# Kernel tuning notes

Measured on AMD Instinct MI355X. Metric: run time of the kernel, lower is better.

## Reference

```python
import jax, jax.numpy as jnp
import numpy as np

LEAK = 0.95
THRESHOLD = 1.0
RESCALE = 2.0


def _xavier_uniform(key, shape, gain=2.0):
    fan_out, fan_in = shape
    bound = gain * np.sqrt(6.0 / (fan_in + fan_out))
    return jax.random.uniform(key, shape, jnp.float32, -bound, bound)


def setup_inputs() -> dict:
    key = jax.random.key(0)
    k_inp, k_w1, k_w2 = jax.random.split(key, 3)
    inp = jax.random.normal(k_inp, (8192, 784), jnp.float32)
    w1 = _xavier_uniform(k_w1, (800, 784))   # fc1.weight
    w2 = _xavier_uniform(k_w2, (10, 800))    # fc2.weight
    return {"inp": inp, "w1": w1, "w2": w2, "num_steps": 25}


@jax.custom_vjp
def spike_fn(x):
    return (x > 0).astype(x.dtype)

def _spike_fwd(x):
    return spike_fn(x), x

def _spike_bwd(x, g):
    # grad = g * 0.3 * relu(1 - |x|)  (surrogate BP)
    return (g * 0.3 * jnp.maximum(1.0 - jnp.abs(x), 0.0),)

spike_fn.defvjp(_spike_fwd, _spike_bwd)


def poisson_gen(key, inp):
    r = jax.random.uniform(key, inp.shape, inp.dtype)
    temp = (r * RESCALE <= jnp.abs(inp)).astype(inp.dtype) * jnp.sign(inp)
    return 0.5 * (temp + 1.0)


def reference(inp, w1, w2, num_steps):
    batch = inp.shape[0]
    x = inp.reshape(batch, -1)
    keys = jax.random.split(jax.random.key(42), num_steps)

    def step(carry, key):
        mem1, mem2 = carry
        sp = poisson_gen(key, x)                    # [B, 784]
        mem1 = LEAK * mem1 + (1.0 - LEAK) * (sp @ w1.T)  # [B, 800]
        mem_thr = mem1 / THRESHOLD - 1.0
        out = spike_fn(mem_thr)
        rst = jnp.where(mem_thr > 0, THRESHOLD, 0.0)
        mem1 = mem1 - jax.lax.stop_gradient(rst)
        mem2 = mem2 + out @ w2.T                    # [B, 10]
        return (mem1, mem2), None

    init = (jnp.zeros((batch, 800), x.dtype), jnp.zeros((batch, 10), x.dtype))
    (_, mem2), _ = jax.lax.scan(step, init, keys)
    return mem2 / num_steps
```

## Files before the change

kernel.cpp:

```cpp
#include <hip/hip_runtime.h>
#include <cstdint>

__host__ __device__ inline uint32_t tf_rotl32(uint32_t x, uint32_t r) {
  return (x << r) | (x >> (32u - r));
}

__host__ __device__ inline void threefry2x32(uint32_t k0, uint32_t k1,
                                             uint32_t x0, uint32_t x1,
                                             uint32_t* o0, uint32_t* o1) {
  uint32_t ks0 = k0, ks1 = k1, ks2 = k0 ^ k1 ^ 0x1BD11BDAu;
  x0 += ks0; x1 += ks1;
#define TF_R(r) { x0 += x1; x1 = tf_rotl32(x1, r); x1 ^= x0; }
  TF_R(13) TF_R(15) TF_R(26) TF_R(6)
  x0 += ks1; x1 += ks2 + 1u;
  TF_R(17) TF_R(29) TF_R(16) TF_R(24)
  x0 += ks2; x1 += ks0 + 2u;
  TF_R(13) TF_R(15) TF_R(26) TF_R(6)
  x0 += ks0; x1 += ks1 + 3u;
  TF_R(17) TF_R(29) TF_R(16) TF_R(24)
  x0 += ks1; x1 += ks2 + 4u;
  TF_R(13) TF_R(15) TF_R(26) TF_R(6)
  x0 += ks2; x1 += ks0 + 5u;
#undef TF_R
  *o0 = x0; *o1 = x1;
}

#define BSZ   8192
#define KIN   784
#define HID   800
#define NOUT  10
#define NSTEP 25


__global__ __launch_bounds__(256) void enc_kernel(const float* __restrict__ inp,
                                                  uint8_t* __restrict__ enc,
                                                  uint32_t k0, uint32_t k1) {
  int j = blockIdx.x * blockDim.x + threadIdx.x;
  if (j >= BSZ * KIN) return;
  uint32_t o0, o1;
  threefry2x32(k0, k1, 0u, (uint32_t)j, &o0, &o1);
  uint32_t bits = o0 ^ o1;
  float r = __uint_as_float((bits >> 9) | 0x3f800000u) - 1.0f;
  float x = inp[j];
  bool cond = (2.0f * r <= fabsf(x));
  int s = (x > 0.0f) ? 1 : ((x < 0.0f) ? -1 : 0);
  enc[j] = (uint8_t)(1 + (cond ? s : 0));
}

__global__ __launch_bounds__(256) void transpose_kernel(const float* __restrict__ w1,
                                                        float* __restrict__ w1t) {
  int idx = blockIdx.x * blockDim.x + threadIdx.x;
  if (idx >= KIN * HID) return;
  int k = idx / HID, n = idx % HID;
  w1t[idx] = w1[(size_t)n * KIN + k];
}

#define BM 512
#define BN 32
#define BK 16

typedef uint32_t u32;

__device__ __forceinline__ float cvt_ub(u32 x, int i) {
  return (float)((x >> (8 * i)) & 0xffu);
}

__device__ __forceinline__ void gload4(const void* g, void* l) {
  __builtin_amdgcn_global_load_lds(
      (const __attribute__((address_space(1))) void*)g,
      (__attribute__((address_space(3))) void*)l, 4, 0, 0);
}

__global__ __launch_bounds__(256) void gemm_kernel(const uint8_t* __restrict__ enc,
                                                   const float* __restrict__ w1t,
                                                   float* __restrict__ gp) {
  __shared__ uint8_t As[2][BM * BK];
  const int panel  = blockIdx.z;
  const int kstart = panel * 264;
  const bool htail = (panel != 2);
  const int m0 = blockIdx.x * BM;
  const int n0 = blockIdx.y * BN;
  const int t  = threadIdx.x;
  const int lane = t & 63;
  const int wv   = t >> 6;

  const uint8_t* a_src = enc + (size_t)(m0 + wv * 128 + (lane >> 2)) * KIN
                         + kstart + (lane & 3) * 4;

  const int r0 = wv * 128 + lane;

  float acc0[32], acc1[32];
#pragma unroll
  for (int c = 0; c < 32; c++) { acc0[c] = 0.0f; acc1[c] = 0.0f; }

#define ISSUE(P, TILE)                                                    \
  {                                                                       \
    _Pragma("unroll")                                                     \
    for (int q = 0; q < 8; q++)                                           \
      gload4(a_src + (size_t)(TILE) * BK + (size_t)(16 * q) * KIN,        \
             &As[P][wv * 2048 + q * 256]);                                \
  }

  ISSUE(0, 0)

  int p = 0;
  for (int tile = 0; tile < 16; tile++) {
    if (tile < 15) { ISSUE(p ^ 1, tile + 1) }
    else if (htail) { ISSUE(p ^ 1, 16) }
    uint4 s0 = *(const uint4*)&As[p][(size_t)r0 * 16];
    uint4 s1 = *(const uint4*)&As[p][(size_t)(r0 + 64) * 16];
    const float* tb = w1t + (size_t)(kstart + tile * BK) * HID + n0;
#pragma unroll
    for (int kk = 0; kk < 16; kk++) {
      const u32 wa0[4] = {s0.x, s0.y, s0.z, s0.w};
      const u32 wa1[4] = {s1.x, s1.y, s1.z, s1.w};
      float a0 = cvt_ub(wa0[kk >> 2], kk & 3);
      float a1 = cvt_ub(wa1[kk >> 2], kk & 3);
      const float* brow = tb + (size_t)kk * HID;
#pragma unroll
      for (int c = 0; c < 32; c++) {
        float b = brow[c];
        acc0[c] = __builtin_fmaf(a0, b, acc0[c]);
        acc1[c] = __builtin_fmaf(a1, b, acc1[c]);
      }
    }
    p ^= 1;
  }
  if (htail) {
    uint4 s0 = *(const uint4*)&As[p][(size_t)r0 * 16];
    uint4 s1 = *(const uint4*)&As[p][(size_t)(r0 + 64) * 16];
    const float* tb = w1t + (size_t)(kstart + 256) * HID + n0;
#pragma unroll
    for (int kk = 0; kk < 8; kk++) {
      const u32 wa0[2] = {s0.x, s0.y};
      const u32 wa1[2] = {s1.x, s1.y};
      float a0 = cvt_ub(wa0[kk >> 2], kk & 3);
      float a1 = cvt_ub(wa1[kk >> 2], kk & 3);
      const float* brow = tb + (size_t)kk * HID;
#pragma unroll
      for (int c = 0; c < 32; c++) {
        float b = brow[c];
        acc0[c] = __builtin_fmaf(a0, b, acc0[c]);
        acc1[c] = __builtin_fmaf(a1, b, acc1[c]);
      }
    }
  }
#undef ISSUE

  const size_t GS = (size_t)BSZ * HID;
  float* o0 = gp + (size_t)panel * GS + (size_t)(m0 + r0) * HID + n0;
  float* o1 = o0 + (size_t)64 * HID;
#pragma unroll
  for (int c = 0; c < 32; c += 4) {
    float4 v0 = {acc0[c], acc0[c + 1], acc0[c + 2], acc0[c + 3]};
    float4 v1 = {acc1[c], acc1[c + 1], acc1[c + 2], acc1[c + 3]};
    *(float4*)(o0 + c) = v0;
    *(float4*)(o1 + c) = v1;
  }
}

__global__ __launch_bounds__(256) void update_kernel(const float* __restrict__ gp,
                                                     float* __restrict__ mem1,
                                                     const float* __restrict__ w2,
                                                     float* __restrict__ mem2) {
  __shared__ float w2s[NOUT * HID];
  for (int i = threadIdx.x; i < NOUT * HID; i += 256) w2s[i] = w2[i];
  __syncthreads();

  const int wave = threadIdx.x / 64;
  const int lane = threadIdx.x % 64;
  const int b = blockIdx.x * 4 + wave;

  const size_t GS = (size_t)BSZ * HID;
  const float* g0 = gp + (size_t)b * HID;
  const float* g1 = g0 + GS;
  const float* g2 = g1 + GS;
  float* mrow = mem1 + (size_t)b * HID;

  float acc[NOUT];
#pragma unroll
  for (int i = 0; i < NOUT; i++) acc[i] = 0.0f;

  for (int j = lane; j < HID; j += 64) {
    float gs = __fmul_rn(0.5f, __fadd_rn(__fadd_rn(g0[j], g1[j]), g2[j]));
    float m = __fadd_rn(__fmul_rn(0.95f, mrow[j]), __fmul_rn(0.05f, gs));
    bool spike = __fadd_rn(m, -1.0f) > 0.0f;
    mrow[j] = spike ? __fadd_rn(m, -1.0f) : m;
    if (spike) {
#pragma unroll
      for (int i = 0; i < NOUT; i++) acc[i] += w2s[i * HID + j];
    }
  }
#pragma unroll
  for (int i = 0; i < NOUT; i++) {
    float v = acc[i];
    for (int off = 32; off > 0; off >>= 1) v += __shfl_down(v, off);
    if (lane == 0) mem2[(size_t)b * NOUT + i] += v;
  }
}

__global__ __launch_bounds__(256) void finalize_kernel(const float* __restrict__ mem2,
                                                       const int* __restrict__ ns,
                                                       float* __restrict__ out) {
  int i = blockIdx.x * blockDim.x + threadIdx.x;
  if (i < BSZ * NOUT) out[i] = mem2[i] / (float)(*ns);
}

extern "C" void kernel_launch(void* const* d_in, const int* in_sizes, int n_in,
                              void* d_out, int out_size, void* d_ws, size_t ws_size,
                              hipStream_t stream) {
  const float* inp = (const float*)d_in[0];
  const float* w1  = (const float*)d_in[1];
  const float* w2  = (const float*)d_in[2];
  const int*   dns = (const int*)d_in[3];
  float* out = (float*)d_out;

  char* ws = (char*)d_ws;
  size_t off = 0;
  uint8_t* enc = (uint8_t*)(ws + off);  off += (size_t)BSZ * KIN;
  off = (off + 255) & ~(size_t)255;
  float* w1t  = (float*)(ws + off);     off += (size_t)KIN * HID * 4;
  float* gp   = (float*)(ws + off);     off += (size_t)3 * BSZ * HID * 4;
  float* mem1 = (float*)(ws + off);     off += (size_t)BSZ * HID * 4;
  float* mem2 = (float*)(ws + off);     off += (size_t)BSZ * NOUT * 4;

  (void)hipMemsetAsync(mem1, 0, (size_t)BSZ * HID * 4, stream);
  (void)hipMemsetAsync(mem2, 0, (size_t)BSZ * NOUT * 4, stream);

  transpose_kernel<<<(KIN * HID + 255) / 256, 256, 0, stream>>>(w1, w1t);

  uint32_t keys[NSTEP][2];
  for (int t = 0; t < NSTEP; t++)
    threefry2x32(0u, 42u, 0u, (uint32_t)t, &keys[t][0], &keys[t][1]);

  const int n_elem = BSZ * KIN;
  for (int t = 0; t < NSTEP; t++) {
    enc_kernel<<<(n_elem + 255) / 256, 256, 0, stream>>>(inp, enc, keys[t][0], keys[t][1]);
    gemm_kernel<<<dim3(BSZ / BM, HID / BN, 3), 256, 0, stream>>>(enc, w1t, gp);
    update_kernel<<<BSZ / 4, 256, 0, stream>>>(gp, mem1, w2, mem2);
  }
  finalize_kernel<<<(BSZ * NOUT + 255) / 256, 256, 0, stream>>>(mem2, dns, out);
}
```

Baseline: 5.348 ms.

## Halve GEMM row tile to one row per thread and pad LDS layout

Shrinks the GEMM M tile from 512 to 256 rows, so each thread accumulates one row of 32 outputs instead of two. This halves accumulator registers to raise occupancy and doubles the grid size. The LDS staging is re-laid out with a padded group stride of 272 bytes so the 16-byte per-lane reads avoid bank conflicts. In exchange, each w1t row load now feeds half as many FMAs, so weight traffic per FLOP doubles.

```diff
diff --git a/kernel.cpp b/kernel.cpp
--- a/kernel.cpp
+++ b/kernel.cpp
@@ -55,9 +55,12 @@
   w1t[idx] = w1[(size_t)n * KIN + k];
 }
 
-#define BM 512
+#define BM 256
 #define BN 32
 #define BK 16
+#define GSTRIDE 272
+#define WSTRIDE (4 * GSTRIDE)
+#define BUFSZ   (4 * WSTRIDE)
 
 typedef uint32_t u32;
 
@@ -74,7 +77,7 @@
 __global__ __launch_bounds__(256) void gemm_kernel(const uint8_t* __restrict__ enc,
                                                    const float* __restrict__ w1t,
                                                    float* __restrict__ gp) {
-  __shared__ uint8_t As[2][BM * BK];
+  __shared__ uint8_t As[2][BUFSZ];
   const int panel  = blockIdx.z;
   const int kstart = panel * 264;
   const bool htail = (panel != 2);
@@ -84,21 +87,22 @@
   const int lane = t & 63;
   const int wv   = t >> 6;
 
-  const uint8_t* a_src = enc + (size_t)(m0 + wv * 128 + (lane >> 2)) * KIN
+  const uint8_t* a_src = enc + (size_t)(m0 + wv * 64 + (lane >> 2)) * KIN
                          + kstart + (lane & 3) * 4;
 
-  const int r0 = wv * 128 + lane;
-
-  float acc0[32], acc1[32];
-#pragma unroll
-  for (int c = 0; c < 32; c++) { acc0[c] = 0.0f; acc1[c] = 0.0f; }
+  const int r0  = wv * 64 + lane;
+  const int ard = wv * WSTRIDE + (lane >> 4) * GSTRIDE + (lane & 15) * 16;
+
+  float acc[32];
+#pragma unroll
+  for (int c = 0; c < 32; c++) acc[c] = 0.0f;
 
 #define ISSUE(P, TILE)                                                    \
   {                                                                       \
     _Pragma("unroll")                                                     \
-    for (int q = 0; q < 8; q++)                                           \
+    for (int q = 0; q < 4; q++)                                           \
       gload4(a_src + (size_t)(TILE) * BK + (size_t)(16 * q) * KIN,        \
-             &As[P][wv * 2048 + q * 256]);                                \
+             &As[P][wv * WSTRIDE + q * GSTRIDE]);                         \
   }
 
   ISSUE(0, 0)
@@ -107,55 +111,40 @@
   for (int tile = 0; tile < 16; tile++) {
     if (tile < 15) { ISSUE(p ^ 1, tile + 1) }
     else if (htail) { ISSUE(p ^ 1, 16) }
-    uint4 s0 = *(const uint4*)&As[p][(size_t)r0 * 16];
-    uint4 s1 = *(const uint4*)&As[p][(size_t)(r0 + 64) * 16];
+    uint4 s0 = *(const uint4*)&As[p][ard];
+    const u32 w[4] = {s0.x, s0.y, s0.z, s0.w};
     const float* tb = w1t + (size_t)(kstart + tile * BK) * HID + n0;
 #pragma unroll
     for (int kk = 0; kk < 16; kk++) {
-      const u32 wa0[4] = {s0.x, s0.y, s0.z, s0.w};
-      const u32 wa1[4] = {s1.x, s1.y, s1.z, s1.w};
-      float a0 = cvt_ub(wa0[kk >> 2], kk & 3);
-      float a1 = cvt_ub(wa1[kk >> 2], kk & 3);
+      float a0 = cvt_ub(w[kk >> 2], kk & 3);
       const float* brow = tb + (size_t)kk * HID;
 #pragma unroll
-      for (int c = 0; c < 32; c++) {
-        float b = brow[c];
-        acc0[c] = __builtin_fmaf(a0, b, acc0[c]);
-        acc1[c] = __builtin_fmaf(a1, b, acc1[c]);
-      }
+      for (int c = 0; c < 32; c++)
+        acc[c] = __builtin_fmaf(a0, brow[c], acc[c]);
     }
     p ^= 1;
   }
   if (htail) {
-    uint4 s0 = *(const uint4*)&As[p][(size_t)r0 * 16];
-    uint4 s1 = *(const uint4*)&As[p][(size_t)(r0 + 64) * 16];
+    uint4 s0 = *(const uint4*)&As[p][ard];
+    const u32 w[2] = {s0.x, s0.y};
     const float* tb = w1t + (size_t)(kstart + 256) * HID + n0;
 #pragma unroll
     for (int kk = 0; kk < 8; kk++) {
-      const u32 wa0[2] = {s0.x, s0.y};
-      const u32 wa1[2] = {s1.x, s1.y};
-      float a0 = cvt_ub(wa0[kk >> 2], kk & 3);
-      float a1 = cvt_ub(wa1[kk >> 2], kk & 3);
+      float a0 = cvt_ub(w[kk >> 2], kk & 3);
       const float* brow = tb + (size_t)kk * HID;
 #pragma unroll
-      for (int c = 0; c < 32; c++) {
-        float b = brow[c];
-        acc0[c] = __builtin_fmaf(a0, b, acc0[c]);
-        acc1[c] = __builtin_fmaf(a1, b, acc1[c]);
-      }
+      for (int c = 0; c < 32; c++)
+        acc[c] = __builtin_fmaf(a0, brow[c], acc[c]);
     }
   }
 #undef ISSUE
 
   const size_t GS = (size_t)BSZ * HID;
   float* o0 = gp + (size_t)panel * GS + (size_t)(m0 + r0) * HID + n0;
-  float* o1 = o0 + (size_t)64 * HID;
 #pragma unroll
   for (int c = 0; c < 32; c += 4) {
-    float4 v0 = {acc0[c], acc0[c + 1], acc0[c + 2], acc0[c + 3]};
-    float4 v1 = {acc1[c], acc1[c + 1], acc1[c + 2], acc1[c + 3]};
+    float4 v0 = {acc[c], acc[c + 1], acc[c + 2], acc[c + 3]};
     *(float4*)(o0 + c) = v0;
-    *(float4*)(o1 + c) = v1;
   }
 }
 
```

Measured after the change: 4.559 ms. -14.8%, faster.
